# Kernel tuning notes

Hardware: AMD Instinct MI355X
Metric: run time of the kernel (lower is better)

## Reference

```python
import jax, jax.numpy as jnp
import numpy as np

N_NODES = 50000
N_EDGES = 600000
IN_DIM = 128
HID_DIM = 128
OUT_DIM = 128
N_GRAPHS = 64


def _glorot(key, shape):
    lim = np.sqrt(6.0 / (shape[0] + shape[1]))
    return jax.random.uniform(key, shape, jnp.float32, -lim, lim)


def setup_inputs() -> dict:
    key = jax.random.key(0)
    ks = jax.random.split(key, 8)
    h = jax.random.normal(ks[0], (N_NODES, IN_DIM), jnp.float32)
    src = jax.random.randint(ks[1], (N_EDGES,), 0, N_NODES, jnp.int64)
    dst = jax.random.randint(ks[2], (N_EDGES,), 0, N_NODES, jnp.int64)
    graph_ids = jnp.sort(jax.random.randint(ks[3], (N_NODES,), 0, N_GRAPHS, jnp.int64))
    W1 = _glorot(ks[4], (IN_DIM, HID_DIM)); b1 = jnp.zeros((HID_DIM,), jnp.float32)
    W2 = _glorot(ks[5], (HID_DIM, HID_DIM)); b2 = jnp.zeros((HID_DIM,), jnp.float32)
    W3 = _glorot(ks[6], (HID_DIM, OUT_DIM)); b3 = jnp.zeros((OUT_DIM,), jnp.float32)
    return {"h": h, "src": src, "dst": dst, "graph_ids": graph_ids,
            "W1": W1, "b1": b1, "W2": W2, "b2": b2, "W3": W3, "b3": b3,
            "n_graphs": N_GRAPHS}


def _graph_conv(h, src, dst, norm_src, norm_dst, W, b):
    # DGL GraphConv, norm='both': D_dst^{-1/2} A^T D_src^{-1/2} h W + b
    m = h * norm_src[:, None]                                   # [N, d]
    agg = jax.ops.segment_sum(m[src], dst, num_segments=h.shape[0])  # [N, d]
    return (agg * norm_dst[:, None]) @ W + b


def reference(h, src, dst, graph_ids, W1, b1, W2, b2, W3, b3, n_graphs):
    n = h.shape[0]
    ones = jnp.ones((src.shape[0],), h.dtype)
    out_deg = jnp.clip(jax.ops.segment_sum(ones, src, num_segments=n), 1.0)
    in_deg = jnp.clip(jax.ops.segment_sum(ones, dst, num_segments=n), 1.0)
    norm_src = out_deg ** -0.5
    norm_dst = in_deg ** -0.5

    x = jax.nn.relu(_graph_conv(h, src, dst, norm_src, norm_dst, W1, b1))
    x = jax.nn.relu(_graph_conv(x, src, dst, norm_src, norm_dst, W2, b2))
    x = jax.nn.relu(_graph_conv(x, src, dst, norm_src, norm_dst, W3, b3))

    # dgl.mean_nodes: per-graph mean over nodes
    gsum = jax.ops.segment_sum(x, graph_ids, num_segments=n_graphs)          # [G, d]
    gcnt = jax.ops.segment_sum(jnp.ones((n,), x.dtype), graph_ids, num_segments=n_graphs)
    return gsum / jnp.clip(gcnt, 1.0)[:, None]
```

## Files before the change

### kernel.cpp

```cpp
#include <hip/hip_runtime.h>
#include <hip/hip_fp16.h>


#define DIM 128

#define HIST_R 4
#define HIST_S 32
#define NPR 12500
#define LDSW (NPR / 2)

__global__ __launch_bounds__(256) void k_hist(const int* __restrict__ src,
                                              const int* __restrict__ dst,
                                              unsigned* __restrict__ partial, int E) {
    __shared__ unsigned hist[LDSW];
    int b = blockIdx.x;
    int a = b / (HIST_R * HIST_S);
    int r = (b / HIST_S) % HIST_R;
    int s = b % HIST_S;
    const int* arr = a ? dst : src;
    for (int i = threadIdx.x; i < LDSW; i += 256) hist[i] = 0;
    __syncthreads();
    int chunk = (E + HIST_S - 1) / HIST_S;
    int e0 = s * chunk;
    int e1 = min(e0 + chunk, E);
    unsigned base = (unsigned)(r * NPR);
    for (int i = e0 + threadIdx.x; i < e1; i += 256) {
        unsigned n = (unsigned)arr[i] - base;
        if (n < NPR) atomicAdd(&hist[n >> 1], 1u << ((n & 1) * 16));
    }
    __syncthreads();
    unsigned* outp = partial + ((size_t)(a * HIST_R + r) * HIST_S + s) * LDSW;
    for (int i = threadIdx.x; i < LDSW; i += 256) outp[i] = hist[i];
}

__global__ void k_hist_merge(const unsigned* __restrict__ partial,
                             float* __restrict__ ns, float* __restrict__ nd,
                             int* __restrict__ inc, int N) {
    int t = blockIdx.x * blockDim.x + threadIdx.x;
    const int total_w = HIST_R * LDSW;
    if (t >= 2 * total_w) return;
    int a = t / total_w;
    int wg = t % total_w;
    int r = wg / LDSW;
    int w = wg % LDSW;
    const unsigned* p = partial + ((size_t)(a * HIST_R + r) * HIST_S) * LDSW + w;
    unsigned sum = 0;
#pragma unroll
    for (int s = 0; s < HIST_S; ++s) sum += p[(size_t)s * LDSW];
    int n0 = r * NPR + w * 2;
    int d0 = (int)(sum & 0xFFFFu);
    int d1 = (int)(sum >> 16);
    if (a == 0) {
        if (n0 < N)     ns[n0]     = rsqrtf(fmaxf((float)d0, 1.0f));
        if (n0 + 1 < N) ns[n0 + 1] = rsqrtf(fmaxf((float)d1, 1.0f));
    } else {
        if (n0 < N)     { nd[n0]     = rsqrtf(fmaxf((float)d0, 1.0f)); inc[n0]     = d0; }
        if (n0 + 1 < N) { nd[n0 + 1] = rsqrtf(fmaxf((float)d1, 1.0f)); inc[n0 + 1] = d1; }
    }
}

__global__ void k_scan_partial(const int* __restrict__ inc, int* __restrict__ bsum, int N) {
    __shared__ int s[256];
    int i = blockIdx.x * 256 + threadIdx.x;
    int t = threadIdx.x;
    s[t] = (i < N) ? inc[i] : 0;
    __syncthreads();
    for (int off = 128; off > 0; off >>= 1) {
        if (t < off) s[t] += s[t + off];
        __syncthreads();
    }
    if (t == 0) bsum[blockIdx.x] = s[0];
}

__global__ void k_scan_top(int* __restrict__ bsum, int nb) {
    __shared__ int s[256];
    int t = threadIdx.x;
    int v = (t < nb) ? bsum[t] : 0;
    s[t] = v;
    __syncthreads();
    for (int off = 1; off < 256; off <<= 1) {
        int u = (t >= off) ? s[t - off] : 0;
        __syncthreads();
        s[t] += u;
        __syncthreads();
    }
    if (t < nb) bsum[t] = s[t] - v;
}

__global__ void k_scan_write(const int* __restrict__ inc, const int* __restrict__ bsum,
                             int* __restrict__ row_ptr, int* __restrict__ cursor, int N) {
    __shared__ int s[256];
    int i = blockIdx.x * 256 + threadIdx.x;
    int t = threadIdx.x;
    int v = (i < N) ? inc[i] : 0;
    s[t] = v;
    __syncthreads();
    for (int off = 1; off < 256; off <<= 1) {
        int u = (t >= off) ? s[t - off] : 0;
        __syncthreads();
        s[t] += u;
        __syncthreads();
    }
    int ex = bsum[blockIdx.x] + s[t] - v;
    if (i < N) { row_ptr[i] = ex; cursor[i] = ex; }
    if (i == N - 1) row_ptr[N] = ex + v;
}

__global__ void k_fill(const int* __restrict__ src, const int* __restrict__ dst,
                       int* __restrict__ cursor, int* __restrict__ csr, int E) {
    int e = blockIdx.x * blockDim.x + threadIdx.x;
    if (e < E) {
        int p = atomicAdd(&cursor[dst[e]], 1);
        csr[p] = src[e];
    }
}

__global__ void k_h2half(const float4* __restrict__ h, const float* __restrict__ ns,
                         uint2* __restrict__ A, int N) {
    int i = blockIdx.x * blockDim.x + threadIdx.x;
    if (i < N * 32) {
        int n = i >> 5;
        float s = ns[n];
        float4 v = h[i];
        __half2 p0 = __floats2half2_rn(v.x * s, v.y * s);
        __half2 p1 = __floats2half2_rn(v.z * s, v.w * s);
        uint2 o;
        o.x = *(unsigned*)&p0;
        o.y = *(unsigned*)&p1;
        A[i] = o;
    }
}

__global__ void k_agg(const uint2* __restrict__ A, const int* __restrict__ row_ptr,
                      const int* __restrict__ csr, const float* __restrict__ nd,
                      float* __restrict__ B, int N) {
    int gtid = blockIdx.x * blockDim.x + threadIdx.x;
    int node = gtid >> 6;
    int lane = threadIdx.x & 63;
    if (node >= N) return;
    int e0 = row_ptr[node];
    int e1 = row_ptr[node + 1];
    int half = lane >> 5;
    int l8 = lane & 31;
    float ax = 0.f, ay = 0.f, az = 0.f, aw = 0.f;

    auto acc4 = [&](uint2 u) {
        __half2 p0 = *(__half2*)&u.x;
        __half2 p1 = *(__half2*)&u.y;
        float2 f0 = __half22float2(p0);
        float2 f1 = __half22float2(p1);
        ax += f0.x; ay += f0.y; az += f1.x; aw += f1.y;
    };

    int e = e0;
    for (; e + 8 <= e1; e += 8) {
        int s0 = csr[e + half];
        int s1 = csr[e + 2 + half];
        int s2 = csr[e + 4 + half];
        int s3 = csr[e + 6 + half];
        uint2 u0 = A[(size_t)s0 * 32 + l8];
        uint2 u1 = A[(size_t)s1 * 32 + l8];
        uint2 u2 = A[(size_t)s2 * 32 + l8];
        uint2 u3 = A[(size_t)s3 * 32 + l8];
        acc4(u0); acc4(u1); acc4(u2); acc4(u3);
    }
    for (; e + 2 <= e1; e += 2) {
        int s0 = csr[e + half];
        acc4(A[(size_t)s0 * 32 + l8]);
    }
    if (e < e1 && half == 0) {
        int s0 = csr[e];
        acc4(A[(size_t)s0 * 32 + l8]);
    }

    ax += __shfl_xor(ax, 32);
    ay += __shfl_xor(ay, 32);
    az += __shfl_xor(az, 32);
    aw += __shfl_xor(aw, 32);

    if (half == 0) {
        float scale = nd[node];
        float4 o;
        o.x = ax * scale; o.y = ay * scale; o.z = az * scale; o.w = aw * scale;
        ((float4*)B)[(size_t)node * 32 + l8] = o;
    }
}

template <bool HALF_OUT>
__global__ __launch_bounds__(256) void k_gemm(
    const float* __restrict__ Y, const float* __restrict__ W,
    const float* __restrict__ bias, const float* __restrict__ ns,
    void* __restrict__ Xout, int N) {
    __shared__ float xsT[32][36];
    __shared__ float ws[32][128];

    int tid = threadIdx.x;
    int tx = tid & 31;
    int ty = tid >> 5;
    int r0 = blockIdx.x * 32;

    float acc[4][4] = {};

    for (int k0 = 0; k0 < 128; k0 += 32) {
        {
            int r = tid >> 3;
            int cq = tid & 7;
            int row = r0 + r;
            float4 v = make_float4(0.f, 0.f, 0.f, 0.f);
            if (row < N) v = *(const float4*)&Y[(size_t)row * DIM + k0 + cq * 4];
            xsT[cq * 4 + 0][r] = v.x;
            xsT[cq * 4 + 1][r] = v.y;
            xsT[cq * 4 + 2][r] = v.z;
            xsT[cq * 4 + 3][r] = v.w;
        }
#pragma unroll
        for (int j = 0; j < 4; ++j) {
            int idx = tid + j * 256;
            int row = idx >> 5;
            int cq = idx & 31;
            *(float4*)&ws[row][cq * 4] =
                *(const float4*)&W[(size_t)(k0 + row) * DIM + cq * 4];
        }
        __syncthreads();
#pragma unroll
        for (int kk = 0; kk < 32; ++kk) {
            float4 a = *(const float4*)&xsT[kk][ty * 4];
            float4 w = *(const float4*)&ws[kk][tx * 4];
            acc[0][0] += a.x * w.x; acc[0][1] += a.x * w.y; acc[0][2] += a.x * w.z; acc[0][3] += a.x * w.w;
            acc[1][0] += a.y * w.x; acc[1][1] += a.y * w.y; acc[1][2] += a.y * w.z; acc[1][3] += a.y * w.w;
            acc[2][0] += a.z * w.x; acc[2][1] += a.z * w.y; acc[2][2] += a.z * w.z; acc[2][3] += a.z * w.w;
            acc[3][0] += a.w * w.x; acc[3][1] += a.w * w.y; acc[3][2] += a.w * w.z; acc[3][3] += a.w * w.w;
        }
        __syncthreads();
    }

    float4 bb = *(const float4*)&bias[tx * 4];
#pragma unroll
    for (int i = 0; i < 4; ++i) {
        int row = r0 + ty * 4 + i;
        if (row >= N) continue;
        float o0 = fmaxf(acc[i][0] + bb.x, 0.0f);
        float o1 = fmaxf(acc[i][1] + bb.y, 0.0f);
        float o2 = fmaxf(acc[i][2] + bb.z, 0.0f);
        float o3 = fmaxf(acc[i][3] + bb.w, 0.0f);
        if (HALF_OUT) {
            float s = ns[row];
            __half2 p0 = __floats2half2_rn(o0 * s, o1 * s);
            __half2 p1 = __floats2half2_rn(o2 * s, o3 * s);
            uint2 o;
            o.x = *(unsigned*)&p0;
            o.y = *(unsigned*)&p1;
            ((uint2*)Xout)[(size_t)row * 32 + tx] = o;
        } else {
            float4 o = make_float4(o0, o1, o2, o3);
            ((float4*)Xout)[(size_t)row * 32 + tx] = o;
        }
    }
}

#define POOL_NODES 32
__global__ void k_pool_partial(const float* __restrict__ X, const int* __restrict__ gid,
                               float* __restrict__ gsum, int* __restrict__ gcnt, int N) {
    int n0 = blockIdx.x * POOL_NODES;
    int d = threadIdx.x;
    int nend = min(n0 + POOL_NODES, N);
    float run = 0.0f;
    int cnt = 0;
    int curg = -1;
    for (int n = n0; n < nend; ++n) {
        int g = gid[n];
        if (g != curg) {
            if (cnt > 0) {
                atomicAdd(&gsum[curg * DIM + d], run);
                if (d == 0) atomicAdd(&gcnt[curg], cnt);
            }
            run = 0.0f; cnt = 0; curg = g;
        }
        run += X[(size_t)n * DIM + d];
        cnt++;
    }
    if (cnt > 0) {
        atomicAdd(&gsum[curg * DIM + d], run);
        if (d == 0) atomicAdd(&gcnt[curg], cnt);
    }
}

__global__ void k_finalize(const float* __restrict__ gsum, const int* __restrict__ gcnt,
                           float* __restrict__ out, int G) {
    int i = blockIdx.x * blockDim.x + threadIdx.x;
    if (i < G * DIM) {
        int g = i >> 7;
        float c = fmaxf((float)gcnt[g], 1.0f);
        out[i] = gsum[i] / c;
    }
}

extern "C" void kernel_launch(void* const* d_in, const int* in_sizes, int n_in,
                              void* d_out, int out_size, void* d_ws, size_t ws_size,
                              hipStream_t stream) {
    const float* h   = (const float*)d_in[0];
    const int*   src = (const int*)d_in[1];
    const int*   dst = (const int*)d_in[2];
    const int*   gid = (const int*)d_in[3];
    const float* W1  = (const float*)d_in[4];
    const float* b1  = (const float*)d_in[5];
    const float* W2  = (const float*)d_in[6];
    const float* b2  = (const float*)d_in[7];
    const float* W3  = (const float*)d_in[8];
    const float* b3  = (const float*)d_in[9];

    const int N = in_sizes[0] / DIM;
    const int E = in_sizes[1];
    const int G = 64;
    float* out = (float*)d_out;

    char* ws = (char*)d_ws;
    size_t off = 0;
    auto alloc = [&](size_t bytes) -> void* {
        void* p = ws + off;
        off += (bytes + 255) & ~(size_t)255;
        return p;
    };
    const int scanBlocks = (N + 255) / 256;
    uint2* Ah      = (uint2*)alloc((size_t)N * DIM * 2);
    float* B       = (float*)alloc((size_t)N * DIM * 4);
    float* X3      = (float*)alloc((size_t)N * DIM * 4);
    float* ns      = (float*)alloc((size_t)N * 4);
    float* nd      = (float*)alloc((size_t)N * 4);
    int*   inc     = (int*)alloc((size_t)N * 4);
    unsigned* partial = (unsigned*)alloc((size_t)2 * HIST_R * HIST_S * LDSW * 4);
    int*   row_ptr = (int*)alloc((size_t)(N + 1) * 4);
    int*   cursor  = (int*)alloc((size_t)N * 4);
    int*   csr     = (int*)alloc((size_t)E * 4);
    float* gsum    = (float*)alloc((size_t)G * DIM * 4);
    int*   gcnt    = (int*)alloc((size_t)G * 4);
    int*   bsum    = (int*)alloc((size_t)scanBlocks * 4);

    hipMemsetAsync(gsum, 0, (size_t)G * DIM * 4, stream);
    hipMemsetAsync(gcnt, 0, (size_t)G * 4, stream);

    k_hist<<<2 * HIST_R * HIST_S, 256, 0, stream>>>(src, dst, partial, E);
    int mergeThreads = 2 * HIST_R * LDSW;
    k_hist_merge<<<(mergeThreads + 255) / 256, 256, 0, stream>>>(partial, ns, nd, inc, N);

    k_scan_partial<<<scanBlocks, 256, 0, stream>>>(inc, bsum, N);
    k_scan_top<<<1, 256, 0, stream>>>(bsum, scanBlocks);
    k_scan_write<<<scanBlocks, 256, 0, stream>>>(inc, bsum, row_ptr, cursor, N);
    k_fill<<<(E + 255) / 256, 256, 0, stream>>>(src, dst, cursor, csr, E);

    int aggBlocks  = (N * 64 + 255) / 256;
    int gemmBlocks = (N + 31) / 32;

    k_h2half<<<(N * 32 + 255) / 256, 256, 0, stream>>>((const float4*)h, ns, Ah, N);
    k_agg<<<aggBlocks, 256, 0, stream>>>(Ah, row_ptr, csr, nd, B, N);
    k_gemm<true><<<gemmBlocks, 256, 0, stream>>>(B, W1, b1, ns, Ah, N);
    k_agg<<<aggBlocks, 256, 0, stream>>>(Ah, row_ptr, csr, nd, B, N);
    k_gemm<true><<<gemmBlocks, 256, 0, stream>>>(B, W2, b2, ns, Ah, N);
    k_agg<<<aggBlocks, 256, 0, stream>>>(Ah, row_ptr, csr, nd, B, N);
    k_gemm<false><<<gemmBlocks, 256, 0, stream>>>(B, W3, b3, ns, X3, N);

    k_pool_partial<<<(N + POOL_NODES - 1) / POOL_NODES, 128, 0, stream>>>(X3, gid, gsum, gcnt, N);
    k_finalize<<<(G * DIM + 255) / 256, 256, 0, stream>>>(gsum, gcnt, out, G);
}
```

Baseline: 346.8 us.

## Fuse neighbor aggregation into GEMM kernel per layer with ping-pong half buffers

Merges the sparse aggregation and the dense 128x128 transform into one kernel per layer. Each block aggregates its 32 rows into shared memory and then multiplies them by W, so the fp32 intermediate B is never written to or read back from global memory. Ping-pong half-precision buffers are added because a layer's output can no longer overwrite the input that other blocks are still gathering from. The cost is fewer concurrent waves per node during aggregation (each wave handles 8 rows in sequence) and more shared memory per block, which may reduce occupancy and latency hiding for the gathers.

```diff
diff --git a/kernel.cpp b/kernel.cpp
--- a/kernel.cpp
+++ b/kernel.cpp
@@ -131,88 +131,76 @@
     }
 }
 
-__global__ void k_agg(const uint2* __restrict__ A, const int* __restrict__ row_ptr,
-                      const int* __restrict__ csr, const float* __restrict__ nd,
-                      float* __restrict__ B, int N) {
-    int gtid = blockIdx.x * blockDim.x + threadIdx.x;
-    int node = gtid >> 6;
-    int lane = threadIdx.x & 63;
-    if (node >= N) return;
-    int e0 = row_ptr[node];
-    int e1 = row_ptr[node + 1];
+template <bool HALF_OUT>
+__global__ __launch_bounds__(256) void k_layer(
+    const uint2* __restrict__ Ain, const int* __restrict__ row_ptr,
+    const int* __restrict__ csr, const float* __restrict__ nd,
+    const float* __restrict__ W, const float* __restrict__ bias,
+    const float* __restrict__ ns, void* __restrict__ Xout, int N) {
+    __shared__ float xsT[DIM][36];
+    __shared__ float ws[32][128];
+
+    int tid = threadIdx.x;
+    int wave = tid >> 6;
+    int lane = tid & 63;
     int half = lane >> 5;
     int l8 = lane & 31;
-    float ax = 0.f, ay = 0.f, az = 0.f, aw = 0.f;
-
-    auto acc4 = [&](uint2 u) {
-        __half2 p0 = *(__half2*)&u.x;
-        __half2 p1 = *(__half2*)&u.y;
-        float2 f0 = __half22float2(p0);
-        float2 f1 = __half22float2(p1);
-        ax += f0.x; ay += f0.y; az += f1.x; aw += f1.y;
-    };
-
-    int e = e0;
-    for (; e + 8 <= e1; e += 8) {
-        int s0 = csr[e + half];
-        int s1 = csr[e + 2 + half];
-        int s2 = csr[e + 4 + half];
-        int s3 = csr[e + 6 + half];
-        uint2 u0 = A[(size_t)s0 * 32 + l8];
-        uint2 u1 = A[(size_t)s1 * 32 + l8];
-        uint2 u2 = A[(size_t)s2 * 32 + l8];
-        uint2 u3 = A[(size_t)s3 * 32 + l8];
-        acc4(u0); acc4(u1); acc4(u2); acc4(u3);
-    }
-    for (; e + 2 <= e1; e += 2) {
-        int s0 = csr[e + half];
-        acc4(A[(size_t)s0 * 32 + l8]);
-    }
-    if (e < e1 && half == 0) {
-        int s0 = csr[e];
-        acc4(A[(size_t)s0 * 32 + l8]);
-    }
-
-    ax += __shfl_xor(ax, 32);
-    ay += __shfl_xor(ay, 32);
-    az += __shfl_xor(az, 32);
-    aw += __shfl_xor(aw, 32);
-
-    if (half == 0) {
-        float scale = nd[node];
-        float4 o;
-        o.x = ax * scale; o.y = ay * scale; o.z = az * scale; o.w = aw * scale;
-        ((float4*)B)[(size_t)node * 32 + l8] = o;
-    }
-}
-
-template <bool HALF_OUT>
-__global__ __launch_bounds__(256) void k_gemm(
-    const float* __restrict__ Y, const float* __restrict__ W,
-    const float* __restrict__ bias, const float* __restrict__ ns,
-    void* __restrict__ Xout, int N) {
-    __shared__ float xsT[32][36];
-    __shared__ float ws[32][128];
-
-    int tid = threadIdx.x;
+    int r0 = blockIdx.x * 32;
+
+    for (int i = 0; i < 8; ++i) {
+        int row = wave * 8 + i;
+        int node = r0 + row;
+        float ax = 0.f, ay = 0.f, az = 0.f, aw = 0.f;
+        if (node < N) {
+            int e0 = row_ptr[node];
+            int e1 = row_ptr[node + 1];
+            auto acc4 = [&](uint2 u) {
+                __half2 p0 = *(__half2*)&u.x;
+                __half2 p1 = *(__half2*)&u.y;
+                float2 f0 = __half22float2(p0);
+                float2 f1 = __half22float2(p1);
+                ax += f0.x; ay += f0.y; az += f1.x; aw += f1.y;
+            };
+            int e = e0;
+            for (; e + 8 <= e1; e += 8) {
+                int s0 = csr[e + half];
+                int s1 = csr[e + 2 + half];
+                int s2 = csr[e + 4 + half];
+                int s3 = csr[e + 6 + half];
+                uint2 u0 = Ain[(size_t)s0 * 32 + l8];
+                uint2 u1 = Ain[(size_t)s1 * 32 + l8];
+                uint2 u2 = Ain[(size_t)s2 * 32 + l8];
+                uint2 u3 = Ain[(size_t)s3 * 32 + l8];
+                acc4(u0); acc4(u1); acc4(u2); acc4(u3);
+            }
+            for (; e + 2 <= e1; e += 2) {
+                int s0 = csr[e + half];
+                acc4(Ain[(size_t)s0 * 32 + l8]);
+            }
+            if (e < e1 && half == 0) {
+                int s0 = csr[e];
+                acc4(Ain[(size_t)s0 * 32 + l8]);
+            }
+        }
+        ax += __shfl_xor(ax, 32);
+        ay += __shfl_xor(ay, 32);
+        az += __shfl_xor(az, 32);
+        aw += __shfl_xor(aw, 32);
+        if (half == 0 && node < N) {
+            float sc = nd[node];
+            xsT[4 * l8 + 0][row] = ax * sc;
+            xsT[4 * l8 + 1][row] = ay * sc;
+            xsT[4 * l8 + 2][row] = az * sc;
+            xsT[4 * l8 + 3][row] = aw * sc;
+        }
+    }
+    __syncthreads();
+
     int tx = tid & 31;
     int ty = tid >> 5;
-    int r0 = blockIdx.x * 32;
-
     float acc[4][4] = {};
 
     for (int k0 = 0; k0 < 128; k0 += 32) {
-        {
-            int r = tid >> 3;
-            int cq = tid & 7;
-            int row = r0 + r;
-            float4 v = make_float4(0.f, 0.f, 0.f, 0.f);
-            if (row < N) v = *(const float4*)&Y[(size_t)row * DIM + k0 + cq * 4];
-            xsT[cq * 4 + 0][r] = v.x;
-            xsT[cq * 4 + 1][r] = v.y;
-            xsT[cq * 4 + 2][r] = v.z;
-            xsT[cq * 4 + 3][r] = v.w;
-        }
 #pragma unroll
         for (int j = 0; j < 4; ++j) {
             int idx = tid + j * 256;
@@ -224,7 +212,7 @@
         __syncthreads();
 #pragma unroll
         for (int kk = 0; kk < 32; ++kk) {
-            float4 a = *(const float4*)&xsT[kk][ty * 4];
+            float4 a = *(const float4*)&xsT[k0 + kk][ty * 4];
             float4 w = *(const float4*)&ws[kk][tx * 4];
             acc[0][0] += a.x * w.x; acc[0][1] += a.x * w.y; acc[0][2] += a.x * w.z; acc[0][3] += a.x * w.w;
             acc[1][0] += a.y * w.x; acc[1][1] += a.y * w.y; acc[1][2] += a.y * w.z; acc[1][3] += a.y * w.w;
@@ -322,8 +310,8 @@
         return p;
     };
     const int scanBlocks = (N + 255) / 256;
-    uint2* Ah      = (uint2*)alloc((size_t)N * DIM * 2);
-    float* B       = (float*)alloc((size_t)N * DIM * 4);
+    uint2* Ah0     = (uint2*)alloc((size_t)N * DIM * 2);
+    uint2* Ah1     = (uint2*)alloc((size_t)N * DIM * 2);
     float* X3      = (float*)alloc((size_t)N * DIM * 4);
     float* ns      = (float*)alloc((size_t)N * 4);
     float* nd      = (float*)alloc((size_t)N * 4);
@@ -348,16 +336,12 @@
     k_scan_write<<<scanBlocks, 256, 0, stream>>>(inc, bsum, row_ptr, cursor, N);
     k_fill<<<(E + 255) / 256, 256, 0, stream>>>(src, dst, cursor, csr, E);
 
-    int aggBlocks  = (N * 64 + 255) / 256;
-    int gemmBlocks = (N + 31) / 32;
-
-    k_h2half<<<(N * 32 + 255) / 256, 256, 0, stream>>>((const float4*)h, ns, Ah, N);
-    k_agg<<<aggBlocks, 256, 0, stream>>>(Ah, row_ptr, csr, nd, B, N);
-    k_gemm<true><<<gemmBlocks, 256, 0, stream>>>(B, W1, b1, ns, Ah, N);
-    k_agg<<<aggBlocks, 256, 0, stream>>>(Ah, row_ptr, csr, nd, B, N);
-    k_gemm<true><<<gemmBlocks, 256, 0, stream>>>(B, W2, b2, ns, Ah, N);
-    k_agg<<<aggBlocks, 256, 0, stream>>>(Ah, row_ptr, csr, nd, B, N);
-    k_gemm<false><<<gemmBlocks, 256, 0, stream>>>(B, W3, b3, ns, X3, N);
+    int layerBlocks = (N + 31) / 32;
+
+    k_h2half<<<(N * 32 + 255) / 256, 256, 0, stream>>>((const float4*)h, ns, Ah0, N);
+    k_layer<true><<<layerBlocks, 256, 0, stream>>>(Ah0, row_ptr, csr, nd, W1, b1, ns, Ah1, N);
+    k_layer<true><<<layerBlocks, 256, 0, stream>>>(Ah1, row_ptr, csr, nd, W2, b2, ns, Ah0, N);
+    k_layer<false><<<layerBlocks, 256, 0, stream>>>(Ah0, row_ptr, csr, nd, W3, b3, ns, X3, N);
 
     k_pool_partial<<<(N + POOL_NODES - 1) / POOL_NODES, 128, 0, stream>>>(X3, gid, gsum, gcnt, N);
     k_finalize<<<(G * DIM + 255) / 256, 256, 0, stream>>>(gsum, gcnt, out, G);
```

After: 434.3 us. 25.2% more time.

## Build CSR using per-chunk histogram cursors and LDS atomics instead of global atomics

Applied to the files above, without the earlier changes.

Replaces the global-atomic CSR fill with a two-step scheme. First, per-(range, chunk) starting cursors are computed from the existing histogram partials plus row_ptr. Then each block places its edge chunk using LDS atomics on a local copy of those cursors, which avoids contended global atomics on cursor[dst]. The histogram chunk count is doubled to give more blocks, and the fp16 activation buffer is double-buffered. The costs are an extra cursor array of about 12.8 MB and 256 fill blocks that each scan a chunk of edges while keeping only the fraction whose dst falls in their range.

```diff
diff --git a/kernel.cpp b/kernel.cpp
--- a/kernel.cpp
+++ b/kernel.cpp
@@ -5,7 +5,7 @@
 #define DIM 128
 
 #define HIST_R 4
-#define HIST_S 32
+#define HIST_S 64
 #define NPR 12500
 #define LDSW (NPR / 2)
 
@@ -88,7 +88,7 @@
 }
 
 __global__ void k_scan_write(const int* __restrict__ inc, const int* __restrict__ bsum,
-                             int* __restrict__ row_ptr, int* __restrict__ cursor, int N) {
+                             int* __restrict__ row_ptr, int N) {
     __shared__ int s[256];
     int i = blockIdx.x * 256 + threadIdx.x;
     int t = threadIdx.x;
@@ -102,16 +102,51 @@
         __syncthreads();
     }
     int ex = bsum[blockIdx.x] + s[t] - v;
-    if (i < N) { row_ptr[i] = ex; cursor[i] = ex; }
+    if (i < N) row_ptr[i] = ex;
     if (i == N - 1) row_ptr[N] = ex + v;
 }
 
-__global__ void k_fill(const int* __restrict__ src, const int* __restrict__ dst,
-                       int* __restrict__ cursor, int* __restrict__ csr, int E) {
-    int e = blockIdx.x * blockDim.x + threadIdx.x;
-    if (e < E) {
-        int p = atomicAdd(&cursor[dst[e]], 1);
-        csr[p] = src[e];
+__global__ void k_cursor(const unsigned* __restrict__ partial, const int* __restrict__ row_ptr,
+                         int* __restrict__ cur, int N) {
+    int t = blockIdx.x * blockDim.x + threadIdx.x;
+    if (t >= HIST_R * LDSW) return;
+    int r = t / LDSW;
+    int w = t % LDSW;
+    int n0 = r * NPR + 2 * w;
+    const unsigned* p = partial + ((size_t)(HIST_R + r) * HIST_S) * LDSW + w;
+    int run0 = (n0 < N) ? row_ptr[n0] : 0;
+    int run1 = (n0 + 1 < N) ? row_ptr[n0 + 1] : 0;
+    int* c = cur + (size_t)r * HIST_S * NPR + 2 * w;
+#pragma unroll
+    for (int s = 0; s < HIST_S; ++s) {
+        c[(size_t)s * NPR + 0] = run0;
+        c[(size_t)s * NPR + 1] = run1;
+        unsigned hv = p[(size_t)s * LDSW];
+        run0 += (int)(hv & 0xFFFFu);
+        run1 += (int)(hv >> 16);
+    }
+}
+
+__global__ __launch_bounds__(256) void k_fill2(const int* __restrict__ src,
+                                               const int* __restrict__ dst,
+                                               const int* __restrict__ cur,
+                                               int* __restrict__ csr, int E) {
+    __shared__ int lcur[NPR];
+    int r = blockIdx.x / HIST_S;
+    int s = blockIdx.x % HIST_S;
+    const int* cs = cur + (size_t)(r * HIST_S + s) * NPR;
+    for (int i = threadIdx.x; i < NPR; i += 256) lcur[i] = cs[i];
+    __syncthreads();
+    int chunk = (E + HIST_S - 1) / HIST_S;
+    int e0 = s * chunk;
+    int e1 = min(e0 + chunk, E);
+    unsigned base = (unsigned)(r * NPR);
+    for (int i = e0 + threadIdx.x; i < e1; i += 256) {
+        unsigned d = (unsigned)dst[i] - base;
+        if (d < NPR) {
+            int p = atomicAdd(&lcur[d], 1);
+            csr[p] = src[i];
+        }
     }
 }
 
@@ -322,15 +357,16 @@
         return p;
     };
     const int scanBlocks = (N + 255) / 256;
-    uint2* Ah      = (uint2*)alloc((size_t)N * DIM * 2);
+    uint2* Ah0     = (uint2*)alloc((size_t)N * DIM * 2);
+    uint2* Ah1     = (uint2*)alloc((size_t)N * DIM * 2);
     float* B       = (float*)alloc((size_t)N * DIM * 4);
     float* X3      = (float*)alloc((size_t)N * DIM * 4);
     float* ns      = (float*)alloc((size_t)N * 4);
     float* nd      = (float*)alloc((size_t)N * 4);
     int*   inc     = (int*)alloc((size_t)N * 4);
     unsigned* partial = (unsigned*)alloc((size_t)2 * HIST_R * HIST_S * LDSW * 4);
+    int*   cur     = (int*)alloc((size_t)HIST_R * HIST_S * NPR * 4);
     int*   row_ptr = (int*)alloc((size_t)(N + 1) * 4);
-    int*   cursor  = (int*)alloc((size_t)N * 4);
     int*   csr     = (int*)alloc((size_t)E * 4);
     float* gsum    = (float*)alloc((size_t)G * DIM * 4);
     int*   gcnt    = (int*)alloc((size_t)G * 4);
@@ -345,18 +381,21 @@
 
     k_scan_partial<<<scanBlocks, 256, 0, stream>>>(inc, bsum, N);
     k_scan_top<<<1, 256, 0, stream>>>(bsum, scanBlocks);
-    k_scan_write<<<scanBlocks, 256, 0, stream>>>(inc, bsum, row_ptr, cursor, N);
-    k_fill<<<(E + 255) / 256, 256, 0, stream>>>(src, dst, cursor, csr, E);
+    k_scan_write<<<scanBlocks, 256, 0, stream>>>(inc, bsum, row_ptr, N);
+
+    int curThreads = HIST_R * LDSW;
+    k_cursor<<<(curThreads + 255) / 256, 256, 0, stream>>>(partial, row_ptr, cur, N);
+    k_fill2<<<HIST_R * HIST_S, 256, 0, stream>>>(src, dst, cur, csr, E);
 
     int aggBlocks  = (N * 64 + 255) / 256;
     int gemmBlocks = (N + 31) / 32;
 
-    k_h2half<<<(N * 32 + 255) / 256, 256, 0, stream>>>((const float4*)h, ns, Ah, N);
-    k_agg<<<aggBlocks, 256, 0, stream>>>(Ah, row_ptr, csr, nd, B, N);
-    k_gemm<true><<<gemmBlocks, 256, 0, stream>>>(B, W1, b1, ns, Ah, N);
-    k_agg<<<aggBlocks, 256, 0, stream>>>(Ah, row_ptr, csr, nd, B, N);
-    k_gemm<true><<<gemmBlocks, 256, 0, stream>>>(B, W2, b2, ns, Ah, N);
-    k_agg<<<aggBlocks, 256, 0, stream>>>(Ah, row_ptr, csr, nd, B, N);
+    k_h2half<<<(N * 32 + 255) / 256, 256, 0, stream>>>((const float4*)h, ns, Ah0, N);
+    k_agg<<<aggBlocks, 256, 0, stream>>>(Ah0, row_ptr, csr, nd, B, N);
+    k_gemm<true><<<gemmBlocks, 256, 0, stream>>>(B, W1, b1, ns, Ah1, N);
+    k_agg<<<aggBlocks, 256, 0, stream>>>(Ah1, row_ptr, csr, nd, B, N);
+    k_gemm<true><<<gemmBlocks, 256, 0, stream>>>(B, W2, b2, ns, Ah0, N);
+    k_agg<<<aggBlocks, 256, 0, stream>>>(Ah0, row_ptr, csr, nd, B, N);
     k_gemm<false><<<gemmBlocks, 256, 0, stream>>>(B, W3, b3, ns, X3, N);
 
     k_pool_partial<<<(N + POOL_NODES - 1) / POOL_NODES, 128, 0, stream>>>(X3, gid, gsum, gcnt, N);
```

New measurement: 336.0 us. -3.1%, faster.
